# Performance work log

Hardware: AMD Instinct MI355X
Metric: run time of the kernel (lower is better)

The kernel has to match this reference:

```python
import jax, jax.numpy as jnp
import numpy as np

B, H, HKV, D, DV, S, M, BN = 16, 32, 8, 128, 128, 8192, 64, 64


def setup_inputs() -> dict:
    key = jax.random.key(0)
    k1, k2, k3, k4 = jax.random.split(key, 4)
    query = jax.random.normal(k1, (B, H, D), dtype=jnp.float32)
    K = jax.random.normal(k2, (B, S, HKV, D), dtype=jnp.float32)
    V = jax.random.normal(k3, (B, S, HKV, DV), dtype=jnp.float32)
    # selected KV block ids per (batch, kv_head); -1 would mean 'skip block'
    block_indices = jax.random.randint(k4, (B, HKV, M), 0, S // BN).astype(jnp.int32)
    cache_seqlens = jnp.full((B,), S, dtype=jnp.int32)
    return {"query": query, "key": K, "value": V,
            "block_indices": block_indices, "cache_seqlens": cache_seqlens,
            "block_size": BN}


def reference(query, key, value, block_indices, cache_seqlens, block_size):
    # query: [B,H,D]  key: [B,S,HKV,D]  value: [B,S,HKV,DV]
    # block_indices: [B,HKV,M] int32 (-1 = invalid)  cache_seqlens: [B] int32
    Bb, Hh, Dd = query.shape
    _, Ss, Hkv, Dv = value.shape
    G = Hh // Hkv  # GQA group size
    scale = 1.0 / np.sqrt(Dd).astype(np.float32)

    valid_blk = block_indices >= 0                              # [B,HKV,M]
    idx = jnp.where(valid_blk, block_indices, 0)
    pos4 = idx[..., None] * block_size + jnp.arange(block_size)  # [B,HKV,M,bn]
    mask4 = valid_blk[..., None] & (pos4 < cache_seqlens[:, None, None, None])
    pos = pos4.reshape(Bb, Hkv, -1)                              # [B,HKV,N] N=M*bn
    mask = mask4.reshape(Bb, Hkv, -1)

    # gather selected KV blocks per (batch, kv_head)
    Kt = key.transpose(0, 2, 1, 3)    # [B,HKV,S,D]
    Vt = value.transpose(0, 2, 1, 3)  # [B,HKV,S,DV]
    Kg = jnp.take_along_axis(Kt, pos[..., None], axis=2)  # [B,HKV,N,D]
    Vg = jnp.take_along_axis(Vt, pos[..., None], axis=2)  # [B,HKV,N,DV]

    q = query.reshape(Bb, Hkv, G, Dd)                      # [B,HKV,G,D]
    s = jnp.einsum('bhgd,bhnd->bhgn', q, Kg) * scale       # [B,HKV,G,N]
    s = jnp.where(mask[:, :, None, :], s, -jnp.inf)
    p = jax.nn.softmax(s, axis=-1)                         # online-softmax equiv.
    o = jnp.einsum('bhgn,bhnd->bhgd', p, Vg)               # [B,HKV,G,DV]
    return o.reshape(Bb, Hh, Dv)
```

## Files before the change

kernel.cpp:

```cpp
#include <hip/hip_runtime.h>
#include <math.h>

#define B_    16
#define H_    32
#define HKV_  8
#define G_    4
#define D_    128
#define DV_   128
#define S_    8192
#define M_    64
#define BN_   64
#define KVSTRIDE (HKV_ * D_)

#define CHUNK_ 32
#define NBLK_  4
#define NC_    (NBLK_ * 2)
#define SPLIT_ (M_ / NBLK_)

__device__ __forceinline__ void gload_lds16(const float* gsrc, float* lds_dst) {
    __builtin_amdgcn_global_load_lds(
        (const __attribute__((address_space(1))) void*)gsrc,
        (__attribute__((address_space(3))) void*)lds_dst,
        16, 0, 0);
}

__device__ __forceinline__ float bcast_lane(float v, int srclane) {
    return __uint_as_float(__builtin_amdgcn_readlane(__float_as_uint(v), srclane));
}

__global__ __launch_bounds__(256)
void sfa_partial(const float* __restrict__ q,
                 const float* __restrict__ K,
                 const float* __restrict__ V,
                 const int*   __restrict__ blk_idx,
                 const int*   __restrict__ seqlens,
                 float* __restrict__ o_ws,
                 float* __restrict__ ml_ws)
{
    __shared__ float Klds[2][CHUNK_ * D_];
    __shared__ float Vlds[2][CHUNK_ * DV_];

    const int wg  = blockIdx.x;
    const int sp  = wg % SPLIT_;
    const int bh  = wg / SPLIT_;
    const int hkv = bh % HKV_;
    const int b   = bh / HKV_;

    const int tid  = threadIdx.x;
    const int wave = tid >> 6;
    const int lane = tid & 63;
    const int c    = lane & 3;
    const int jr   = lane >> 2;

    const int h = hkv * G_ + wave;
    const float kscale = 0.08838834764831845f * 1.4426950408889634f;

    float4 q4[8];
    {
        const float* qp = q + (size_t)(b * H_ + h) * D_ + c * 4;
        #pragma unroll
        for (int f = 0; f < 8; ++f) {
            float4 t = *(const float4*)(qp + f * 16);
            q4[f] = make_float4(t.x * kscale, t.y * kscale,
                                t.z * kscale, t.w * kscale);
        }
    }

    const int seqlen = seqlens[b];
    int blks[NBLK_];
    {
        const int* bip = blk_idx + (b * HKV_ + hkv) * M_ + sp * NBLK_;
        #pragma unroll
        for (int i = 0; i < NBLK_; ++i) blks[i] = bip[i];
    }

    const float* Kb = K + (size_t)b * S_ * KVSTRIDE + hkv * D_;
    const float* Vb = V + (size_t)b * S_ * KVSTRIDE + hkv * D_;

    asm volatile("s_waitcnt vmcnt(0)" ::: "memory");

    auto stageK = [&](int ci) {
        const int blk  = blks[ci >> 1];
        const int blkc = (blk < 0) ? 0 : blk;
        const size_t rowbase = (size_t)blkc * BN_ + (ci & 1) * CHUNK_;
        float* dst = &Klds[ci & 1][0];
        #pragma unroll
        for (int i = 0; i < 4; ++i) {
            const int p   = wave * 4 + i;
            const int row = 2 * p + (lane >> 5);
            const int g16 = lane & 31;
            const float* src = Kb + (rowbase + row) * KVSTRIDE
                                  + ((g16 ^ (row & 7)) << 2);
            gload_lds16(src, dst + p * 256);
        }
    };
    auto stageV = [&](int ci) {
        const int blk  = blks[ci >> 1];
        const int blkc = (blk < 0) ? 0 : blk;
        const size_t rowbase = (size_t)blkc * BN_ + (ci & 1) * CHUNK_;
        float* dst = &Vlds[ci & 1][0];
        #pragma unroll
        for (int i = 0; i < 4; ++i) {
            const int p   = wave * 4 + i;
            const int row = 2 * p + (lane >> 5);
            const int g16 = lane & 31;
            const float* src = Vb + (rowbase + row) * KVSTRIDE + (g16 << 2);
            gload_lds16(src, dst + p * 256);
        }
    };

    float m  = -INFINITY;
    float l  = 0.f;
    float o0 = 0.f, o1 = 0.f;

    stageK(0); stageV(0); stageK(1);

    #pragma unroll
    for (int ci = 0; ci < NC_; ++ci) {
        const int blk    = blks[ci >> 1];
        const bool bval  = (blk >= 0);
        const int  pos0  = ((blk < 0) ? 0 : blk) * BN_ + (ci & 1) * CHUNK_;

        if (ci < NC_ - 1) asm volatile("s_waitcnt vmcnt(8)" ::: "memory");
        else              asm volatile("s_waitcnt vmcnt(4)" ::: "memory");
        __builtin_amdgcn_s_barrier();
        __builtin_amdgcn_sched_barrier(0);

        float s[2];
        #pragma unroll
        for (int bt = 0; bt < 2; ++bt) {
            const int r = bt * 16 + jr;
            const float* kr = &Klds[ci & 1][r * D_];
            float acc = 0.f;
            #pragma unroll
            for (int f = 0; f < 8; ++f) {
                const int gg = (((f * 4 + c) ^ (r & 7)) << 2);
                float4 k4 = *(const float4*)(kr + gg);
                acc += q4[f].x * k4.x;
                acc += q4[f].y * k4.y;
                acc += q4[f].z * k4.z;
                acc += q4[f].w * k4.w;
            }
            acc += __shfl_xor(acc, 1);
            acc += __shfl_xor(acc, 2);
            s[bt] = (bval && (pos0 + r) < seqlen) ? acc : -INFINITY;
        }

        if (ci + 1 < NC_) stageV(ci + 1);

        if (ci < NC_ - 1) asm volatile("s_waitcnt vmcnt(8)" ::: "memory");
        else              asm volatile("s_waitcnt vmcnt(0)" ::: "memory");
        __builtin_amdgcn_s_barrier();
        __builtin_amdgcn_sched_barrier(0);

        if (ci + 2 < NC_) stageK(ci + 2);

        float bmax = fmaxf(s[0], s[1]);
        #pragma unroll
        for (int off = 4; off < 64; off <<= 1)
            bmax = fmaxf(bmax, __shfl_xor(bmax, off));

        const float newm = fmaxf(m, bmax);
        if (newm != -INFINITY) {
            const float rr = __builtin_amdgcn_exp2f(m - newm);
            const float p0 = __builtin_amdgcn_exp2f(s[0] - newm);
            const float p1 = __builtin_amdgcn_exp2f(s[1] - newm);
            float ps = p0 + p1;
            #pragma unroll
            for (int off = 4; off < 64; off <<= 1)
                ps += __shfl_xor(ps, off);

            l  = l * rr + ps;
            o0 *= rr;
            o1 *= rr;
            m  = newm;

            const float* vp0 = &Vlds[ci & 1][lane * 2];
            #pragma unroll
            for (int jj = 0; jj < 16; ++jj) {
                const float pj = bcast_lane(p0, jj * 4);
                const float2 v2 = *(const float2*)(vp0 + jj * DV_);
                o0 += pj * v2.x;
                o1 += pj * v2.y;
            }
            #pragma unroll
            for (int jj = 0; jj < 16; ++jj) {
                const float pj = bcast_lane(p1, jj * 4);
                const float2 v2 = *(const float2*)(vp0 + (16 + jj) * DV_);
                o0 += pj * v2.x;
                o1 += pj * v2.y;
            }
        }
    }

    const int pidx = (bh * G_ + wave) * SPLIT_ + sp;
    o_ws[(size_t)pidx * DV_ + lane * 2]     = o0;
    o_ws[(size_t)pidx * DV_ + lane * 2 + 1] = o1;
    if (lane == 0) {
        ml_ws[pidx * 2]     = m;
        ml_ws[pidx * 2 + 1] = l;
    }
}

template<int SPLIT>
__global__ __launch_bounds__(64)
void sfa_reduce(const float* __restrict__ o_ws,
                const float* __restrict__ ml_ws,
                float* __restrict__ out)
{
    const int bhg  = blockIdx.x;
    const int lane = threadIdx.x;

    float mi = -INFINITY, li = 0.f;
    if (lane < SPLIT) {
        const float2 t = ((const float2*)ml_ws)[bhg * SPLIT + lane];
        mi = t.x; li = t.y;
    }
    float mfull = mi;
    #pragma unroll
    for (int off = 1; off < 64; off <<= 1)
        mfull = fmaxf(mfull, __shfl_xor(mfull, off));

    const float f = (mi == -INFINITY) ? 0.f
                  : __builtin_amdgcn_exp2f(mi - mfull);
    float L = li * f;
    #pragma unroll
    for (int off = 1; off < 64; off <<= 1)
        L += __shfl_xor(L, off);

    float o0 = 0.f, o1 = 0.f;
    #pragma unroll
    for (int i = 0; i < SPLIT; ++i) {
        const float fi = bcast_lane(f, i);
        if (fi != 0.f) {
            const float* op = o_ws + (size_t)(bhg * SPLIT + i) * DV_ + lane * 2;
            o0 += fi * op[0];
            o1 += fi * op[1];
        }
    }
    const float inv = (L > 0.f) ? (1.f / L) : 0.f;
    out[(size_t)bhg * DV_ + lane * 2]     = o0 * inv;
    out[(size_t)bhg * DV_ + lane * 2 + 1] = o1 * inv;
}

extern "C" void kernel_launch(void* const* d_in, const int* in_sizes, int n_in,
                              void* d_out, int out_size, void* d_ws, size_t ws_size,
                              hipStream_t stream) {
    const float* q    = (const float*)d_in[0];
    const float* K    = (const float*)d_in[1];
    const float* V    = (const float*)d_in[2];
    const int*   bidx = (const int*)d_in[3];
    const int*   slen = (const int*)d_in[4];

    float* o_ws  = (float*)d_ws;
    float* ml_ws = o_ws + (size_t)B_ * HKV_ * G_ * SPLIT_ * DV_;

    sfa_partial<<<B_ * HKV_ * SPLIT_, 256, 0, stream>>>(
        q, K, V, bidx, slen, o_ws, ml_ws);

    sfa_reduce<SPLIT_><<<B_ * H_, 64, 0, stream>>>(o_ws, ml_ws, (float*)d_out);
}
```

Measured before the change: 98.01 us.

## Process four split items per workgroup with a continuous cross-item prefetch pipeline

Each workgroup now handles four consecutive splits of a (batch, kv-head) pair instead of one. The K/V double-buffered prefetch pipeline continues across item boundaries, so it is not refilled from scratch per split, and the q load and setup are amortized. Block indices are loaded once into lanes and broadcast with readlane. The workgroup-to-(b,hkv) mapping is also remapped. The grid shrinks from 2048 to 512 workgroups, which lowers parallelism and occupancy headroom on a 256-CU device in exchange for less per-workgroup startup cost.

```diff
diff --git a/kernel.cpp b/kernel.cpp
--- a/kernel.cpp
+++ b/kernel.cpp
@@ -14,8 +14,9 @@
 
 #define CHUNK_ 32
 #define NBLK_  4
-#define NC_    (NBLK_ * 2)
 #define SPLIT_ (M_ / NBLK_)
+#define ITEMS_ 4
+#define NCTOT_ (ITEMS_ * NBLK_ * 2)
 
 __device__ __forceinline__ void gload_lds16(const float* gsrc, float* lds_dst) {
     __builtin_amdgcn_global_load_lds(
@@ -40,11 +41,12 @@
     __shared__ float Klds[2][CHUNK_ * D_];
     __shared__ float Vlds[2][CHUNK_ * DV_];
 
-    const int wg  = blockIdx.x;
-    const int sp  = wg % SPLIT_;
-    const int bh  = wg / SPLIT_;
-    const int hkv = bh % HKV_;
-    const int b   = bh / HKV_;
+    const int w    = blockIdx.x;
+    const int t    = w >> 3;
+    const int bh   = (w & 7) + 8 * (t & 15);
+    const int quad = t >> 4;
+    const int hkv  = bh & 7;
+    const int b    = bh >> 3;
 
     const int tid  = threadIdx.x;
     const int wave = tid >> 6;
@@ -60,30 +62,25 @@
         const float* qp = q + (size_t)(b * H_ + h) * D_ + c * 4;
         #pragma unroll
         for (int f = 0; f < 8; ++f) {
-            float4 t = *(const float4*)(qp + f * 16);
-            q4[f] = make_float4(t.x * kscale, t.y * kscale,
-                                t.z * kscale, t.w * kscale);
-        }
-    }
+            float4 tq = *(const float4*)(qp + f * 16);
+            q4[f] = make_float4(tq.x * kscale, tq.y * kscale,
+                                tq.z * kscale, tq.w * kscale);
+        }
+    }
+
+    int vblk = 0;
+    if (lane < 16) vblk = blk_idx[bh * M_ + quad * 16 + lane];
 
     const int seqlen = seqlens[b];
-    int blks[NBLK_];
-    {
-        const int* bip = blk_idx + (b * HKV_ + hkv) * M_ + sp * NBLK_;
-        #pragma unroll
-        for (int i = 0; i < NBLK_; ++i) blks[i] = bip[i];
-    }
-
     const float* Kb = K + (size_t)b * S_ * KVSTRIDE + hkv * D_;
     const float* Vb = V + (size_t)b * S_ * KVSTRIDE + hkv * D_;
 
     asm volatile("s_waitcnt vmcnt(0)" ::: "memory");
 
-    auto stageK = [&](int ci) {
-        const int blk  = blks[ci >> 1];
+    auto stageK = [&](int cc, int blk) {
         const int blkc = (blk < 0) ? 0 : blk;
-        const size_t rowbase = (size_t)blkc * BN_ + (ci & 1) * CHUNK_;
-        float* dst = &Klds[ci & 1][0];
+        const size_t rowbase = (size_t)blkc * BN_ + (cc & 1) * CHUNK_;
+        float* dst = &Klds[cc & 1][0];
         #pragma unroll
         for (int i = 0; i < 4; ++i) {
             const int p   = wave * 4 + i;
@@ -94,11 +91,10 @@
             gload_lds16(src, dst + p * 256);
         }
     };
-    auto stageV = [&](int ci) {
-        const int blk  = blks[ci >> 1];
+    auto stageV = [&](int cc, int blk) {
         const int blkc = (blk < 0) ? 0 : blk;
-        const size_t rowbase = (size_t)blkc * BN_ + (ci & 1) * CHUNK_;
-        float* dst = &Vlds[ci & 1][0];
+        const size_t rowbase = (size_t)blkc * BN_ + (cc & 1) * CHUNK_;
+        float* dst = &Vlds[cc & 1][0];
         #pragma unroll
         for (int i = 0; i < 4; ++i) {
             const int p   = wave * 4 + i;
@@ -108,97 +104,109 @@
             gload_lds16(src, dst + p * 256);
         }
     };
+    auto blkOf = [&](int cc) -> int {
+        return __builtin_amdgcn_readlane(vblk, cc >> 1);
+    };
 
     float m  = -INFINITY;
     float l  = 0.f;
     float o0 = 0.f, o1 = 0.f;
 
-    stageK(0); stageV(0); stageK(1);
-
-    #pragma unroll
-    for (int ci = 0; ci < NC_; ++ci) {
-        const int blk    = blks[ci >> 1];
-        const bool bval  = (blk >= 0);
-        const int  pos0  = ((blk < 0) ? 0 : blk) * BN_ + (ci & 1) * CHUNK_;
-
-        if (ci < NC_ - 1) asm volatile("s_waitcnt vmcnt(8)" ::: "memory");
-        else              asm volatile("s_waitcnt vmcnt(4)" ::: "memory");
-        __builtin_amdgcn_s_barrier();
-        __builtin_amdgcn_sched_barrier(0);
-
-        float s[2];
-        #pragma unroll
-        for (int bt = 0; bt < 2; ++bt) {
-            const int r = bt * 16 + jr;
-            const float* kr = &Klds[ci & 1][r * D_];
-            float acc = 0.f;
+    stageK(0, blkOf(0));
+    stageV(0, blkOf(0));
+    stageK(1, blkOf(1));
+
+    #pragma unroll 1
+    for (int item = 0; item < ITEMS_; ++item) {
+        #pragma unroll
+        for (int ci = 0; ci < 8; ++ci) {
+            const int  cc   = item * 8 + ci;
+            const int  blk  = blkOf(cc);
+            const bool bval = (blk >= 0);
+            const int  pos0 = ((blk < 0) ? 0 : blk) * BN_ + (cc & 1) * CHUNK_;
+            const bool last = (cc == NCTOT_ - 1);
+
+            if (last) asm volatile("s_waitcnt vmcnt(4)" ::: "memory");
+            else      asm volatile("s_waitcnt vmcnt(8)" ::: "memory");
+            __builtin_amdgcn_s_barrier();
+            __builtin_amdgcn_sched_barrier(0);
+
+            float s[2];
             #pragma unroll
-            for (int f = 0; f < 8; ++f) {
-                const int gg = (((f * 4 + c) ^ (r & 7)) << 2);
-                float4 k4 = *(const float4*)(kr + gg);
-                acc += q4[f].x * k4.x;
-                acc += q4[f].y * k4.y;
-                acc += q4[f].z * k4.z;
-                acc += q4[f].w * k4.w;
+            for (int bt = 0; bt < 2; ++bt) {
+                const int r = bt * 16 + jr;
+                const float* kr = &Klds[cc & 1][r * D_];
+                float acc = 0.f;
+                #pragma unroll
+                for (int f = 0; f < 8; ++f) {
+                    const int gg = (((f * 4 + c) ^ (r & 7)) << 2);
+                    float4 k4 = *(const float4*)(kr + gg);
+                    acc += q4[f].x * k4.x;
+                    acc += q4[f].y * k4.y;
+                    acc += q4[f].z * k4.z;
+                    acc += q4[f].w * k4.w;
+                }
+                acc += __shfl_xor(acc, 1);
+                acc += __shfl_xor(acc, 2);
+                s[bt] = (bval && (pos0 + r) < seqlen) ? acc : -INFINITY;
             }
-            acc += __shfl_xor(acc, 1);
-            acc += __shfl_xor(acc, 2);
-            s[bt] = (bval && (pos0 + r) < seqlen) ? acc : -INFINITY;
-        }
-
-        if (ci + 1 < NC_) stageV(ci + 1);
-
-        if (ci < NC_ - 1) asm volatile("s_waitcnt vmcnt(8)" ::: "memory");
-        else              asm volatile("s_waitcnt vmcnt(0)" ::: "memory");
-        __builtin_amdgcn_s_barrier();
-        __builtin_amdgcn_sched_barrier(0);
-
-        if (ci + 2 < NC_) stageK(ci + 2);
-
-        float bmax = fmaxf(s[0], s[1]);
-        #pragma unroll
-        for (int off = 4; off < 64; off <<= 1)
-            bmax = fmaxf(bmax, __shfl_xor(bmax, off));
-
-        const float newm = fmaxf(m, bmax);
-        if (newm != -INFINITY) {
-            const float rr = __builtin_amdgcn_exp2f(m - newm);
-            const float p0 = __builtin_amdgcn_exp2f(s[0] - newm);
-            const float p1 = __builtin_amdgcn_exp2f(s[1] - newm);
-            float ps = p0 + p1;
+
+            if (cc + 1 < NCTOT_) stageV(cc + 1, blkOf(cc + 1));
+
+            if (last) asm volatile("s_waitcnt vmcnt(0)" ::: "memory");
+            else      asm volatile("s_waitcnt vmcnt(8)" ::: "memory");
+            __builtin_amdgcn_s_barrier();
+            __builtin_amdgcn_sched_barrier(0);
+
+            if (cc + 2 < NCTOT_) stageK(cc + 2, blkOf(cc + 2));
+
+            float bmax = fmaxf(s[0], s[1]);
             #pragma unroll
             for (int off = 4; off < 64; off <<= 1)
-                ps += __shfl_xor(ps, off);
-
-            l  = l * rr + ps;
-            o0 *= rr;
-            o1 *= rr;
-            m  = newm;
-
-            const float* vp0 = &Vlds[ci & 1][lane * 2];
-            #pragma unroll
-            for (int jj = 0; jj < 16; ++jj) {
-                const float pj = bcast_lane(p0, jj * 4);
-                const float2 v2 = *(const float2*)(vp0 + jj * DV_);
-                o0 += pj * v2.x;
-                o1 += pj * v2.y;
+                bmax = fmaxf(bmax, __shfl_xor(bmax, off));
+
+            const float newm = fmaxf(m, bmax);
+            if (newm != -INFINITY) {
+                const float rr = __builtin_amdgcn_exp2f(m - newm);
+                const float p0 = __builtin_amdgcn_exp2f(s[0] - newm);
+                const float p1 = __builtin_amdgcn_exp2f(s[1] - newm);
+                float ps = p0 + p1;
+                #pragma unroll
+                for (int off = 4; off < 64; off <<= 1)
+                    ps += __shfl_xor(ps, off);
+
+                l  = l * rr + ps;
+                o0 *= rr;
+                o1 *= rr;
+                m  = newm;
+
+                const float* vp0 = &Vlds[cc & 1][lane * 2];
+                #pragma unroll
+                for (int jj = 0; jj < 16; ++jj) {
+                    const float pj = bcast_lane(p0, jj * 4);
+                    const float2 v2 = *(const float2*)(vp0 + jj * DV_);
+                    o0 += pj * v2.x;
+                    o1 += pj * v2.y;
+                }
+                #pragma unroll
+                for (int jj = 0; jj < 16; ++jj) {
+                    const float pj = bcast_lane(p1, jj * 4);
+                    const float2 v2 = *(const float2*)(vp0 + (16 + jj) * DV_);
+                    o0 += pj * v2.x;
+                    o1 += pj * v2.y;
+                }
             }
-            #pragma unroll
-            for (int jj = 0; jj < 16; ++jj) {
-                const float pj = bcast_lane(p1, jj * 4);
-                const float2 v2 = *(const float2*)(vp0 + (16 + jj) * DV_);
-                o0 += pj * v2.x;
-                o1 += pj * v2.y;
+
+            if (ci == 7) {
+                const int sp   = quad * ITEMS_ + item;
+                const int pidx = (bh * G_ + wave) * SPLIT_ + sp;
+                *(float2*)(o_ws + (size_t)pidx * DV_ + lane * 2) =
+                    make_float2(o0, o1);
+                if (lane == 0)
+                    *(float2*)(ml_ws + pidx * 2) = make_float2(m, l);
+                m = -INFINITY; l = 0.f; o0 = 0.f; o1 = 0.f;
             }
         }
-    }
-
-    const int pidx = (bh * G_ + wave) * SPLIT_ + sp;
-    o_ws[(size_t)pidx * DV_ + lane * 2]     = o0;
-    o_ws[(size_t)pidx * DV_ + lane * 2 + 1] = o1;
-    if (lane == 0) {
-        ml_ws[pidx * 2]     = m;
-        ml_ws[pidx * 2 + 1] = l;
     }
 }
 
@@ -255,7 +263,7 @@
     float* o_ws  = (float*)d_ws;
     float* ml_ws = o_ws + (size_t)B_ * HKV_ * G_ * SPLIT_ * DV_;
 
-    sfa_partial<<<B_ * HKV_ * SPLIT_, 256, 0, stream>>>(
+    sfa_partial<<<B_ * HKV_ * SPLIT_ / ITEMS_, 256, 0, stream>>>(
         q, K, V, bidx, slen, o_ws, ml_ws);
 
     sfa_reduce<SPLIT_><<<B_ * H_, 64, 0, stream>>>(o_ws, ml_ws, (float*)d_out);
```

Result: faster. 93.64 us (-4.5%).
